# Performance work log

Measured on AMD Instinct MI355X. Metric: run time of the kernel, lower is better.

## Reference

```python
import jax, jax.numpy as jnp
import numpy as np

ROUTER_TEMP = 1.0
ALPHA = 1.0
EPS = 1e-6


def _rmsnorm(x, w):
    var = jnp.mean(x * x, axis=-1, keepdims=True)
    return x * jax.lax.rsqrt(var + EPS) * w


def _block(x, wg, wu, wd, nw):
    # stand-in recursion block: residual RMSNorm + SwiGLU MLP (pointwise over tokens)
    xn = _rmsnorm(x, nw)
    return x + (jax.nn.silu(xn @ wg) * (xn @ wu)) @ wd


def setup_inputs() -> dict:
    key = jax.random.key(0)
    ks = jax.random.split(key, 5)
    B, S, D, F, L = 2, 4096, 2048, 8192, 2
    return {
        "hidden_states": jax.random.normal(ks[0], (B, S, D), jnp.float32),
        "router_w": jax.random.normal(ks[1], (L, D), jnp.float32) * 0.02,
        "Wg": jax.random.normal(ks[2], (L, D, F), jnp.float32) * (D ** -0.5),
        "Wu": jax.random.normal(ks[3], (L, D, F), jnp.float32) * (D ** -0.5),
        "Wd": jax.random.normal(ks[4], (L, F, D), jnp.float32) * (F ** -0.5),
        "norm_w": jnp.ones((L, D), jnp.float32),
    }


def reference(hidden_states, router_w, Wg, Wu, Wd, norm_w):
    L = router_w.shape[0]
    # router: logits (B,S,L), softmax probs scaled by alpha, top-1 routing
    router_logits = (hidden_states / ROUTER_TEMP) @ router_w.T
    router_probs = jax.nn.softmax(router_logits, axis=-1) * ALPHA
    idx = jnp.argmax(router_probs, axis=-1)                      # (B,S)
    weights = jnp.take_along_axis(router_probs, idx[..., None], axis=-1)  # (B,S,1)
    # run every level's block densely on all tokens (pointwise blocks =>
    # identical math to original gather/pad/compute/scatter), then select
    y = jax.vmap(_block, in_axes=(None, 0, 0, 0, 0))(hidden_states, Wg, Wu, Wd, norm_w)  # (L,B,S,D)
    onehot = jax.nn.one_hot(idx, L, dtype=hidden_states.dtype)   # (B,S,L)
    sel = jnp.einsum("lbsd,bsl->bsd", y, onehot)
    output = hidden_states + weights * sel                       # gating == 'weighted'
    # router z-loss: mean of squared logsumexp over levels
    z = jax.nn.logsumexp(router_logits, axis=-1)
    router_z_loss = jnp.mean(z * z)
    return output, router_z_loss
```

## Files before the change

kernel.cpp:

```cpp
#include <hip/hip_runtime.h>
#include <hip/hip_bf16.h>
#include <stdint.h>

#define B_    2
#define S_    4096
#define D_    2048
#define F_    8192
#define L_    2
#define FQ    (F_ / 4)
#define NTOK  (B_ * S_)
#define RCAP  (NTOK + 128)
#define EPS_  1e-6f

typedef __attribute__((ext_vector_type(8))) short s16x8;
typedef __attribute__((ext_vector_type(4))) float f32x4;

typedef unsigned short u16;
typedef unsigned int   u32;

#define OFF_CNT   ((size_t)0)
#define OFF_ZL    ((size_t)128)
#define OFF_MAP   ((size_t)384)
#define OFF_WROW  ((size_t)33664)
#define OFF_WTOK  ((size_t)66944)
#define OFF_XG    ((size_t)99712)
#define OFF_HQ    ((size_t)34178432)
#define OFF_WA    ((size_t)68257152)
#define OFF_WB    ((size_t)85034368)

__device__ __forceinline__ u16 f2bf(float f) {
    u32 u = __builtin_bit_cast(u32, f);
    u += 0x7fff + ((u >> 16) & 1);
    return (u16)(u >> 16);
}

__device__ __forceinline__ void gl16(const u16* g, u16* l) {
    __builtin_amdgcn_global_load_lds(
        (const __attribute__((address_space(1))) void*)g,
        (__attribute__((address_space(3))) void*)l, 16, 0, 0);
}

#define MF(acc, va, vb) acc = __builtin_amdgcn_mfma_f32_16x16x32_bf16(va, vb, acc, 0, 0, 0)

__global__ void k_init(int* counts, float* zacc) {
    if (threadIdx.x == 0) { counts[0] = 0; counts[16] = 0; }
    zacc[threadIdx.x & 63] = 0.f;
}

__global__ __launch_bounds__(256) void k_router(
    const float* __restrict__ hs, const float* __restrict__ rw,
    const float* __restrict__ nw, int* __restrict__ counts,
    float* __restrict__ zacc, int* __restrict__ tmap,
    float* __restrict__ wrow, float* __restrict__ wtok, u16* __restrict__ Xg)
{
    int t = blockIdx.x;
    int tid = threadIdx.x;
    const float* x = hs + (size_t)t * D_;
    float xs[8];
    float sxx = 0.f, s0 = 0.f, s1 = 0.f;
#pragma unroll
    for (int i = 0; i < 8; i++) {
        int d = tid + i * 256;
        float v = x[d];
        xs[i] = v;
        sxx += v * v;
        s0  += v * rw[d];
        s1  += v * rw[D_ + d];
    }
#pragma unroll
    for (int off = 32; off; off >>= 1) {
        sxx += __shfl_down(sxx, off, 64);
        s0  += __shfl_down(s0,  off, 64);
        s1  += __shfl_down(s1,  off, 64);
    }
    __shared__ float red[3][4];
    __shared__ float bcf[1];
    __shared__ int   bci[2];
    int wave = tid >> 6, lane = tid & 63;
    if (lane == 0) { red[0][wave] = sxx; red[1][wave] = s0; red[2][wave] = s1; }
    __syncthreads();
    if (tid == 0) {
        sxx = red[0][0] + red[0][1] + red[0][2] + red[0][3];
        s0  = red[1][0] + red[1][1] + red[1][2] + red[1][3];
        s1  = red[2][0] + red[2][1] + red[2][2] + red[2][3];
        float m  = fmaxf(s0, s1);
        float e0 = __expf(s0 - m), e1 = __expf(s1 - m);
        float Z  = e0 + e1;
        int   idx = (s1 > s0) ? 1 : 0;
        float p   = ((idx == 0) ? e0 : e1) / Z;
        float z   = m + __logf(Z);
        atomicAdd(&zacc[t & 63], z * z * (1.0f / NTOK));
        int pos = atomicAdd(&counts[idx << 4], 1);
        int row = (idx == 0) ? pos : (RCAP - 1 - pos);
        tmap[row] = t;
        wrow[row] = p;
        wtok[t]   = p;
        bcf[0] = rsqrtf(sxx * (1.0f / D_) + EPS_);
        bci[0] = idx; bci[1] = row;
    }
    __syncthreads();
    float inv = bcf[0];
    int idx = bci[0], row = bci[1];
    u16* xr = Xg + (size_t)row * D_;
    const float* w = nw + (size_t)idx * D_;
#pragma unroll
    for (int i = 0; i < 8; i++) {
        int d = tid + i * 256;
        xr[d] = f2bf(xs[i] * inv * w[d]);
    }
}

__global__ __launch_bounds__(256) void k_gap(const int* counts, int* tmap, u16* Xg) {
    int row = counts[0] + blockIdx.x;
    uint4* p = (uint4*)(Xg + (size_t)row * D_);
    p[threadIdx.x] = make_uint4(0u, 0u, 0u, 0u);
    if (threadIdx.x == 0) tmap[row] = -1;
}

__global__ __launch_bounds__(256) void k_outinit(
    const float* __restrict__ hs, const float* __restrict__ wtok,
    float* __restrict__ out)
{
    int t = blockIdx.x;
    float c = 1.f + wtok[t];
    const float4* ip = (const float4*)(hs + (size_t)t * D_);
    float4* op = (float4*)(out + (size_t)t * D_);
#pragma unroll
    for (int i = 0; i < 2; i++) {
        float4 v = ip[threadIdx.x + i * 256];
        v.x *= c; v.y *= c; v.z *= c; v.w *= c;
        op[threadIdx.x + i * 256] = v;
    }
}

__global__ __launch_bounds__(256) void k_transposeGU(
    const float* __restrict__ Wg, const float* __restrict__ Wu,
    u16* __restrict__ WA, u16* __restrict__ WB, int c0)
{
    __shared__ float tile[32][33];
    int z = blockIdx.z;
    int m = z & 1, lvl = z >> 1;
    const float* ip = (m ? Wu : Wg) + (size_t)lvl * D_ * F_;
    u16* op = (m ? WB : WA) + (size_t)lvl * FQ * D_;
    int lc0 = blockIdx.x * 32;
    int lr0 = blockIdx.y * 32;
    int tx = threadIdx.x & 31, ty = threadIdx.x >> 5;
#pragma unroll
    for (int i = 0; i < 4; i++)
        tile[ty + i * 8][tx] = ip[(size_t)(lr0 + ty + i * 8) * F_ + (c0 + lc0 + tx)];
    __syncthreads();
#pragma unroll
    for (int i = 0; i < 4; i++)
        op[(size_t)(lc0 + ty + i * 8) * D_ + lr0 + tx] = f2bf(tile[tx][ty + i * 8]);
}

__global__ __launch_bounds__(256) void k_transpose(
    const float* __restrict__ in, u16* __restrict__ out,
    int R, int C, int r0, int c0, int RL, int CL)
{
    __shared__ float tile[32][33];
    int lc0 = blockIdx.x * 32;
    int lr0 = blockIdx.y * 32;
    const float* ip = in + (size_t)blockIdx.z * (size_t)R * (size_t)C;
    u16* op = out + (size_t)blockIdx.z * (size_t)CL * (size_t)RL;
    int tx = threadIdx.x & 31, ty = threadIdx.x >> 5;
#pragma unroll
    for (int i = 0; i < 4; i++)
        tile[ty + i * 8][tx] = ip[(size_t)(r0 + lr0 + ty + i * 8) * C + (c0 + lc0 + tx)];
    __syncthreads();
#pragma unroll
    for (int i = 0; i < 4; i++)
        op[(size_t)(lc0 + ty + i * 8) * RL + lr0 + tx] = f2bf(tile[tx][ty + i * 8]);
}

__global__ __launch_bounds__(256, 3) void k_gemm1(
    const u16* __restrict__ Xg, const u16* __restrict__ WgT,
    const u16* __restrict__ WuT, const int* __restrict__ counts,
    u16* __restrict__ Hq)
{
    int nt = blockIdx.x, mt = blockIdx.y;
    int count0 = counts[0];
    int level = (mt * 128 < count0) ? 0 : 1;
    const u16* Bg = WgT + (size_t)level * FQ * D_;
    const u16* Bu = WuT + (size_t)level * FQ * D_;

    __shared__ __align__(16) u16 As[8192 + 6144];
    __shared__ __align__(16) u16 Gs[4096], Us[4096];

    int tid = threadIdx.x, lane = tid & 63, wave = tid >> 6;
    int wm = wave >> 1, wn = wave & 1;
    int quad = lane >> 4, ln = lane & 15;
    int swz = ln & 7;

    f32x4 accG[4][2] = {}, accU[4][2] = {};

    int srow = tid >> 3;
    int sswz = ((tid & 7) ^ (srow & 7)) * 8;
    const u16* gA = Xg + (size_t)(mt * 128 + srow) * D_ + sswz;
    const u16* gG = Bg + (size_t)(nt * 64 + srow) * D_ + sswz;
    const u16* gU = Bu + (size_t)(nt * 64 + srow) * D_ + sswz;
    u16* dA = As + wave * 512;
    u16* dG = Gs + wave * 512;
    u16* dU = Us + wave * 512;

    for (int k0 = 0; k0 < D_; k0 += 64) {
        __syncthreads();
        gl16(gA + k0, dA);
        gl16(gA + (size_t)32 * D_ + k0, dA + 2048);
        gl16(gA + (size_t)64 * D_ + k0, dA + 4096);
        gl16(gA + (size_t)96 * D_ + k0, dA + 6144);
        gl16(gG + k0, dG);
        gl16(gG + (size_t)32 * D_ + k0, dG + 2048);
        gl16(gU + k0, dU);
        gl16(gU + (size_t)32 * D_ + k0, dU + 2048);
        __syncthreads();
#pragma unroll
        for (int h = 0; h < 2; ++h) {
            int ks = ((h * 4 + quad) ^ swz) * 8;
            s16x8 a[4], bg[2], bu[2];
#pragma unroll
            for (int i = 0; i < 4; ++i)
                a[i] = *(const s16x8*)(As + (wm * 64 + i * 16 + ln) * 64 + ks);
#pragma unroll
            for (int j = 0; j < 2; ++j) {
                bg[j] = *(const s16x8*)(Gs + (wn * 32 + j * 16 + ln) * 64 + ks);
                bu[j] = *(const s16x8*)(Us + (wn * 32 + j * 16 + ln) * 64 + ks);
            }
#pragma unroll
            for (int mi = 0; mi < 4; ++mi)
#pragma unroll
                for (int j = 0; j < 2; ++j) {
                    MF(accG[mi][j], a[mi], bg[j]);
                    MF(accU[mi][j], a[mi], bu[j]);
                }
        }
    }

    int rowbase = mt * 128 + wm * 64;
    int colbase = nt * 64 + wn * 32;
#pragma unroll
    for (int mi = 0; mi < 4; ++mi)
#pragma unroll
        for (int j = 0; j < 2; ++j)
#pragma unroll
            for (int r = 0; r < 4; ++r) {
                float g = accG[mi][j][r], u = accU[mi][j][r];
                float h = g / (1.f + __expf(-g)) * u;
                int row = rowbase + mi * 16 + quad * 4 + r;
                int col = colbase + j * 16 + ln;
                Hq[(size_t)row * FQ + col] = f2bf(h);
            }
}

__global__ __launch_bounds__(256, 3) void k_gemm2(
    const u16* __restrict__ Hq, const u16* __restrict__ WdT,
    const int* __restrict__ counts, const int* __restrict__ tmap,
    const float* __restrict__ wrow, float* __restrict__ out)
{
    int nt = blockIdx.x, mt = blockIdx.y;
    int count0 = counts[0];
    int level = (mt * 128 < count0) ? 0 : 1;
    const u16* Bd = WdT + (size_t)level * D_ * FQ;

    __shared__ __align__(16) u16 As[8192 + 9728];
    __shared__ __align__(16) u16 Bs[4096];
    __shared__ int   stok[128];
    __shared__ float sw[128];

    int tid = threadIdx.x, lane = tid & 63, wave = tid >> 6;
    int wm = wave >> 1, wn = wave & 1;
    int quad = lane >> 4, ln = lane & 15;
    int swz = ln & 7;

    if (tid < 128) { stok[tid] = tmap[mt * 128 + tid]; sw[tid] = wrow[mt * 128 + tid]; }

    f32x4 acc[4][2] = {};

    int srow = tid >> 3;
    int sswz = ((tid & 7) ^ (srow & 7)) * 8;
    const u16* gA = Hq + (size_t)(mt * 128 + srow) * FQ + sswz;
    const u16* gB = Bd + (size_t)(nt * 64 + srow) * FQ + sswz;
    u16* dA = As + wave * 512;
    u16* dB = Bs + wave * 512;

    for (int k0 = 0; k0 < FQ; k0 += 64) {
        __syncthreads();
        gl16(gA + k0, dA);
        gl16(gA + (size_t)32 * FQ + k0, dA + 2048);
        gl16(gA + (size_t)64 * FQ + k0, dA + 4096);
        gl16(gA + (size_t)96 * FQ + k0, dA + 6144);
        gl16(gB + k0, dB);
        gl16(gB + (size_t)32 * FQ + k0, dB + 2048);
        __syncthreads();
#pragma unroll
        for (int h = 0; h < 2; ++h) {
            int ks = ((h * 4 + quad) ^ swz) * 8;
            s16x8 a[4], b[2];
#pragma unroll
            for (int i = 0; i < 4; ++i)
                a[i] = *(const s16x8*)(As + (wm * 64 + i * 16 + ln) * 64 + ks);
#pragma unroll
            for (int j = 0; j < 2; ++j)
                b[j] = *(const s16x8*)(Bs + (wn * 32 + j * 16 + ln) * 64 + ks);
#pragma unroll
            for (int mi = 0; mi < 4; ++mi)
#pragma unroll
                for (int j = 0; j < 2; ++j)
                    MF(acc[mi][j], a[mi], b[j]);
        }
    }

    int colbase = nt * 64 + wn * 32;
#pragma unroll
    for (int mi = 0; mi < 4; ++mi)
#pragma unroll
        for (int j = 0; j < 2; ++j)
#pragma unroll
            for (int r = 0; r < 4; ++r) {
                int rl = wm * 64 + mi * 16 + quad * 4 + r;
                int tok = stok[rl];
                if (tok < 0) continue;
                int col = colbase + j * 16 + ln;
                out[(size_t)tok * D_ + col] += sw[rl] * acc[mi][j][r];
            }
}

__global__ void k_zout(const float* zacc, float* out) {
    float s = 0.f;
#pragma unroll
    for (int i = 0; i < 64; i++) s += zacc[i];
    out[(size_t)NTOK * D_] = s;
}

extern "C" void kernel_launch(void* const* d_in, const int* in_sizes, int n_in,
                              void* d_out, int out_size, void* d_ws, size_t ws_size,
                              hipStream_t stream) {
    const float* hs = (const float*)d_in[0];
    const float* rw = (const float*)d_in[1];
    const float* Wg = (const float*)d_in[2];
    const float* Wu = (const float*)d_in[3];
    const float* Wd = (const float*)d_in[4];
    const float* nw = (const float*)d_in[5];
    float* out = (float*)d_out;

    char* ws = (char*)d_ws;
    int*   counts = (int*)(ws + OFF_CNT);
    float* zacc   = (float*)(ws + OFF_ZL);
    int*   tmap   = (int*)(ws + OFF_MAP);
    float* wrow   = (float*)(ws + OFF_WROW);
    float* wtok   = (float*)(ws + OFF_WTOK);
    u16*   Xg     = (u16*)(ws + OFF_XG);
    u16*   Hq     = (u16*)(ws + OFF_HQ);
    u16*   WA     = (u16*)(ws + OFF_WA);
    u16*   WB     = (u16*)(ws + OFF_WB);

    k_init<<<1, 64, 0, stream>>>(counts, zacc);
    k_router<<<NTOK, 256, 0, stream>>>(hs, rw, nw, counts, zacc, tmap, wrow, wtok, Xg);
    k_gap<<<128, 256, 0, stream>>>(counts, tmap, Xg);
    k_outinit<<<NTOK, 256, 0, stream>>>(hs, wtok, out);

    for (int q = 0; q < 4; q++) {
        k_transposeGU<<<dim3(FQ / 32, D_ / 32, 2 * L_), 256, 0, stream>>>(Wg, Wu, WA, WB, q * FQ);
        k_gemm1<<<dim3(FQ / 64, RCAP / 128), 256, 0, stream>>>(Xg, WA, WB, counts, Hq);
        k_transpose<<<dim3(D_ / 32, FQ / 32, L_), 256, 0, stream>>>(Wd, WA, F_, D_, q * FQ, 0, FQ, D_);
        k_gemm2<<<dim3(D_ / 64, RCAP / 128), 256, 0, stream>>>(Hq, WA, counts, tmap, wrow, out);
    }
    k_zout<<<1, 1, 0, stream>>>(zacc, out);
}
```

Measured before the change: 1.561 ms.

## Pipeline both GEMM mainloops with a triple-buffered LDS ring and K=32 stages

Both GEMM kernels now use a 3-stage LDS ring with K-tiles of 32 instead of a single buffer with K=64. Global-to-LDS loads for tile t+2 are issued while tile t is computed, synchronised by manual vmcnt waits and one barrier per iteration instead of two __syncthreads. The swizzle is changed to fit the 32-wide rows, and s_setprio raises wave priority around the MFMA block. The intent is to hide load latency and cut barrier stalls. In exchange the code depends on hand-placed waitcnt counts and uses a different LDS footprint, which may change occupancy.

```diff
diff --git a/kernel.cpp b/kernel.cpp
--- a/kernel.cpp
+++ b/kernel.cpp
@@ -184,57 +184,64 @@
     const u16* Bg = WgT + (size_t)level * FQ * D_;
     const u16* Bu = WuT + (size_t)level * FQ * D_;
 
-    __shared__ __align__(16) u16 As[8192 + 6144];
-    __shared__ __align__(16) u16 Gs[4096], Us[4096];
+    __shared__ __align__(16) u16 lds[3 * 8192];
 
     int tid = threadIdx.x, lane = tid & 63, wave = tid >> 6;
     int wm = wave >> 1, wn = wave & 1;
     int quad = lane >> 4, ln = lane & 15;
-    int swz = ln & 7;
+    int rswz = (quad ^ ((ln >> 1) & 3)) * 8;
 
     f32x4 accG[4][2] = {}, accU[4][2] = {};
 
-    int srow = tid >> 3;
-    int sswz = ((tid & 7) ^ (srow & 7)) * 8;
+    int srow = tid >> 2;
+    int sswz = ((tid & 3) ^ ((tid >> 3) & 3)) * 8;
     const u16* gA = Xg + (size_t)(mt * 128 + srow) * D_ + sswz;
     const u16* gG = Bg + (size_t)(nt * 64 + srow) * D_ + sswz;
     const u16* gU = Bu + (size_t)(nt * 64 + srow) * D_ + sswz;
-    u16* dA = As + wave * 512;
-    u16* dG = Gs + wave * 512;
-    u16* dU = Us + wave * 512;
-
-    for (int k0 = 0; k0 < D_; k0 += 64) {
-        __syncthreads();
-        gl16(gA + k0, dA);
-        gl16(gA + (size_t)32 * D_ + k0, dA + 2048);
-        gl16(gA + (size_t)64 * D_ + k0, dA + 4096);
-        gl16(gA + (size_t)96 * D_ + k0, dA + 6144);
-        gl16(gG + k0, dG);
-        gl16(gG + (size_t)32 * D_ + k0, dG + 2048);
-        gl16(gU + k0, dU);
-        gl16(gU + (size_t)32 * D_ + k0, dU + 2048);
-        __syncthreads();
-#pragma unroll
-        for (int h = 0; h < 2; ++h) {
-            int ks = ((h * 4 + quad) ^ swz) * 8;
-            s16x8 a[4], bg[2], bu[2];
-#pragma unroll
-            for (int i = 0; i < 4; ++i)
-                a[i] = *(const s16x8*)(As + (wm * 64 + i * 16 + ln) * 64 + ks);
+    int wb = wave * 512;
+
+#define STAGE1(kt, b) do { \
+        u16* base_ = lds + (b) * 8192; int k_ = (kt) * 32; \
+        gl16(gA + k_, base_ + wb); \
+        gl16(gA + (size_t)64 * D_ + k_, base_ + 2048 + wb); \
+        gl16(gG + k_, base_ + 4096 + wb); \
+        gl16(gU + k_, base_ + 6144 + wb); \
+    } while (0)
+
+    STAGE1(0, 0);
+    STAGE1(1, 1);
+    asm volatile("s_waitcnt vmcnt(4)" ::: "memory");
+    asm volatile("s_barrier" ::: "memory");
+
+    int cur = 0;
+    for (int t = 0; t < 64; ++t) {
+        const u16* As = lds + cur * 8192;
+        int stg = cur + 2; if (stg >= 3) stg -= 3;
+        if (t + 2 < 64) STAGE1(t + 2, stg);
+        s16x8 a[4], bg[2], bu[2];
+#pragma unroll
+        for (int i = 0; i < 4; ++i)
+            a[i] = *(const s16x8*)(As + (wm * 64 + i * 16 + ln) * 32 + rswz);
+#pragma unroll
+        for (int j = 0; j < 2; ++j) {
+            bg[j] = *(const s16x8*)(As + 4096 + (wn * 32 + j * 16 + ln) * 32 + rswz);
+            bu[j] = *(const s16x8*)(As + 6144 + (wn * 32 + j * 16 + ln) * 32 + rswz);
+        }
+        __builtin_amdgcn_s_setprio(1);
+#pragma unroll
+        for (int mi = 0; mi < 4; ++mi)
 #pragma unroll
             for (int j = 0; j < 2; ++j) {
-                bg[j] = *(const s16x8*)(Gs + (wn * 32 + j * 16 + ln) * 64 + ks);
-                bu[j] = *(const s16x8*)(Us + (wn * 32 + j * 16 + ln) * 64 + ks);
+                MF(accG[mi][j], a[mi], bg[j]);
+                MF(accU[mi][j], a[mi], bu[j]);
             }
-#pragma unroll
-            for (int mi = 0; mi < 4; ++mi)
-#pragma unroll
-                for (int j = 0; j < 2; ++j) {
-                    MF(accG[mi][j], a[mi], bg[j]);
-                    MF(accU[mi][j], a[mi], bu[j]);
-                }
-        }
-    }
+        __builtin_amdgcn_s_setprio(0);
+        if (t < 62)       { asm volatile("s_waitcnt vmcnt(4)" ::: "memory"); }
+        else if (t == 62) { asm volatile("s_waitcnt vmcnt(0)" ::: "memory"); }
+        if (t < 63) asm volatile("s_barrier" ::: "memory");
+        cur = cur + 1; if (cur == 3) cur = 0;
+    }
+#undef STAGE1
 
     int rowbase = mt * 128 + wm * 64;
     int colbase = nt * 64 + wn * 32;
@@ -262,53 +269,62 @@
     int level = (mt * 128 < count0) ? 0 : 1;
     const u16* Bd = WdT + (size_t)level * D_ * FQ;
 
-    __shared__ __align__(16) u16 As[8192 + 9728];
-    __shared__ __align__(16) u16 Bs[4096];
+    __shared__ __align__(16) u16 lds[3 * 6144 + 6144];
     __shared__ int   stok[128];
     __shared__ float sw[128];
 
     int tid = threadIdx.x, lane = tid & 63, wave = tid >> 6;
     int wm = wave >> 1, wn = wave & 1;
     int quad = lane >> 4, ln = lane & 15;
-    int swz = ln & 7;
+    int rswz = (quad ^ ((ln >> 1) & 3)) * 8;
 
     if (tid < 128) { stok[tid] = tmap[mt * 128 + tid]; sw[tid] = wrow[mt * 128 + tid]; }
 
     f32x4 acc[4][2] = {};
 
-    int srow = tid >> 3;
-    int sswz = ((tid & 7) ^ (srow & 7)) * 8;
+    int srow = tid >> 2;
+    int sswz = ((tid & 3) ^ ((tid >> 3) & 3)) * 8;
     const u16* gA = Hq + (size_t)(mt * 128 + srow) * FQ + sswz;
     const u16* gB = Bd + (size_t)(nt * 64 + srow) * FQ + sswz;
-    u16* dA = As + wave * 512;
-    u16* dB = Bs + wave * 512;
-
-    for (int k0 = 0; k0 < FQ; k0 += 64) {
-        __syncthreads();
-        gl16(gA + k0, dA);
-        gl16(gA + (size_t)32 * FQ + k0, dA + 2048);
-        gl16(gA + (size_t)64 * FQ + k0, dA + 4096);
-        gl16(gA + (size_t)96 * FQ + k0, dA + 6144);
-        gl16(gB + k0, dB);
-        gl16(gB + (size_t)32 * FQ + k0, dB + 2048);
-        __syncthreads();
-#pragma unroll
-        for (int h = 0; h < 2; ++h) {
-            int ks = ((h * 4 + quad) ^ swz) * 8;
-            s16x8 a[4], b[2];
-#pragma unroll
-            for (int i = 0; i < 4; ++i)
-                a[i] = *(const s16x8*)(As + (wm * 64 + i * 16 + ln) * 64 + ks);
+    int wb = wave * 512;
+
+#define STAGE2(kt, b) do { \
+        u16* base_ = lds + (b) * 6144; int k_ = (kt) * 32; \
+        gl16(gA + k_, base_ + wb); \
+        gl16(gA + (size_t)64 * FQ + k_, base_ + 2048 + wb); \
+        gl16(gB + k_, base_ + 4096 + wb); \
+    } while (0)
+
+    STAGE2(0, 0);
+    STAGE2(1, 1);
+    asm volatile("s_waitcnt vmcnt(3)" ::: "memory");
+    asm volatile("s_barrier" ::: "memory");
+
+    int cur = 0;
+    for (int t = 0; t < 64; ++t) {
+        const u16* As = lds + cur * 6144;
+        int stg = cur + 2; if (stg >= 3) stg -= 3;
+        if (t + 2 < 64) STAGE2(t + 2, stg);
+        s16x8 a[4], b[2];
+#pragma unroll
+        for (int i = 0; i < 4; ++i)
+            a[i] = *(const s16x8*)(As + (wm * 64 + i * 16 + ln) * 32 + rswz);
+#pragma unroll
+        for (int j = 0; j < 2; ++j)
+            b[j] = *(const s16x8*)(As + 4096 + (wn * 32 + j * 16 + ln) * 32 + rswz);
+        __builtin_amdgcn_s_setprio(1);
+#pragma unroll
+        for (int mi = 0; mi < 4; ++mi)
 #pragma unroll
             for (int j = 0; j < 2; ++j)
-                b[j] = *(const s16x8*)(Bs + (wn * 32 + j * 16 + ln) * 64 + ks);
-#pragma unroll
-            for (int mi = 0; mi < 4; ++mi)
-#pragma unroll
-                for (int j = 0; j < 2; ++j)
-                    MF(acc[mi][j], a[mi], b[j]);
-        }
-    }
+                MF(acc[mi][j], a[mi], b[j]);
+        __builtin_amdgcn_s_setprio(0);
+        if (t < 62)       { asm volatile("s_waitcnt vmcnt(3)" ::: "memory"); }
+        else if (t == 62) { asm volatile("s_waitcnt vmcnt(0)" ::: "memory"); }
+        if (t < 63) asm volatile("s_barrier" ::: "memory");
+        cur = cur + 1; if (cur == 3) cur = 0;
+    }
+#undef STAGE2
 
     int colbase = nt * 64 + wn * 32;
 #pragma unroll
```

New measurement: 1.789 ms. 14.6% more time.
